# Kernel optimization log

Measured on AMD Instinct MI355X. Metric: run time of the kernel, lower is better.

The kernel has to match this reference:

```python
import jax, jax.numpy as jnp
import numpy as np

B, K, D = 32768, 32, 128

def setup_inputs() -> dict:
    key = jax.random.key(0)
    k1, k2, k3, k4, k5, k6 = jax.random.split(key, 6)
    s = 1.0 / np.sqrt(D)
    return {
        "h_ego": jax.random.normal(k1, (B, D), jnp.float32),
        "h_nei": jax.random.normal(k2, (B, K, D), jnp.float32),
        "nbr_mask": jax.random.randint(k3, (B, K), 0, 2, jnp.int32),
        "W_msg": jax.random.normal(k4, (D, D), jnp.float32) * s,
        "W_attn": jax.random.normal(k5, (1, 2 * D), jnp.float32) * s,
        "W_self": jax.random.normal(k6, (D, D), jnp.float32) * s,
        "b_self": jnp.zeros((D,), jnp.float32),
    }

def reference(h_ego, h_nei, nbr_mask, W_msg, W_attn, W_self, b_self):
    # msg_proj (nn.Linear, no bias): y = x @ W.T
    nbr_proj = jnp.einsum('bkd,ed->bke', h_nei, W_msg)          # [B,K,D]
    ego_proj = jnp.einsum('bd,ed->be', h_ego, W_msg)            # [B,D]
    # additive scorer on [ego_proj || nbr_proj]: split W_attn into two halves
    a = W_attn[0]                                               # [2D]
    a_ego, a_nbr = a[:D], a[D:]
    logits = ego_proj @ a_ego[:, None]                          # [B,1]
    logits = logits + jnp.einsum('bkd,d->bk', nbr_proj, a_nbr)  # [B,K]
    logits = jax.nn.leaky_relu(logits, negative_slope=0.2)
    logits = jnp.where(nbr_mask > 0, logits, -jnp.inf)
    attn = jax.nn.softmax(logits, axis=1)                       # [B,K]
    attn = jnp.where(jnp.isfinite(attn), attn, 0.0)
    nbr_message = jnp.einsum('bkd,bk->bd', nbr_proj, attn)      # [B,D]
    self_loop = h_ego @ W_self.T + b_self                       # [B,D]
    return jnp.tanh(nbr_message + self_loop)
```

## Files before the change

kernel.cpp:

```cpp
#include <hip/hip_runtime.h>
#include <hip/hip_bf16.h>
#include <math.h>

#define B_ROWS 32768
#define KNBR 32
#define DDIM 128

#define WS_VEGO 0
#define WS_VNBR 128
#define WS_WMT  256
#define WS_WST  (256 + 128*128)

__global__ __launch_bounds__(256) void prep_kernel(
    const float* __restrict__ W_msg, const float* __restrict__ W_attn,
    const float* __restrict__ W_self, float* __restrict__ ws) {
    int t = threadIdx.x;
    int gid = blockIdx.x * 256 + t;
    if (gid < 128 * 128) {
        int e = gid >> 7, d = gid & 127;
        ws[WS_WMT + d * 128 + e] = W_msg[e * 128 + d];
        ws[WS_WST + d * 128 + e] = W_self[e * 128 + d];
    }
    if (blockIdx.x == 0 && t < 128) {
        float ve = 0.f, vn = 0.f;
        for (int e = 0; e < 128; ++e) {
            float w = W_msg[e * 128 + t];
            ve += W_attn[e] * w;
            vn += W_attn[128 + e] * w;
        }
        ws[WS_VEGO + t] = ve;
        ws[WS_VNBR + t] = vn;
    }
}

__global__ __launch_bounds__(256) void attn_kernel(
    const float* __restrict__ h_ego, const float* __restrict__ h_nei,
    const int* __restrict__ nbr_mask, const float* __restrict__ ws,
    float* __restrict__ hbar_out) {
    __shared__ float hn[KNBR * DDIM];
    __shared__ float he[DDIM];
    __shared__ float sve[DDIM];
    __shared__ float svn[DDIM];
    __shared__ float s_raw[KNBR];
    __shared__ float s_attn[KNBR];
    __shared__ float s_ego;

    int t = threadIdx.x;
    long b = blockIdx.x;

    const float4* src = (const float4*)(h_nei + b * (KNBR * DDIM));
    float4* dst = (float4*)hn;
#pragma unroll
    for (int i = 0; i < 4; ++i) dst[i * 256 + t] = src[i * 256 + t];
    if (t < 32) {
        ((float4*)he)[t] = ((const float4*)(h_ego + b * DDIM))[t];
    } else if (t < 64) {
        ((float4*)sve)[t - 32] = ((const float4*)(ws + WS_VEGO))[t - 32];
    } else if (t < 96) {
        ((float4*)svn)[t - 64] = ((const float4*)(ws + WS_VNBR))[t - 64];
    }
    __syncthreads();

    int w = t >> 6, l = t & 63;

    if (w == 0) {
        float p = he[l] * sve[l] + he[l + 64] * sve[l + 64];
#pragma unroll
        for (int s = 32; s; s >>= 1) p += __shfl_xor(p, s, 64);
        if (l == 0) s_ego = p;
    }
#pragma unroll
    for (int j = 0; j < 8; ++j) {
        int k = w * 8 + j;
        const float* row = hn + k * DDIM;
        float p = row[l] * svn[l] + row[l + 64] * svn[l + 64];
#pragma unroll
        for (int s = 32; s; s >>= 1) p += __shfl_xor(p, s, 64);
        if (l == 0) s_raw[k] = p;
    }
    __syncthreads();

    if (w == 0) {
        float logit = -INFINITY;
        bool valid = false;
        if (l < KNBR) {
            float x = s_raw[l] + s_ego;
            x = x > 0.f ? x : 0.2f * x;
            valid = nbr_mask[b * KNBR + l] > 0;
            logit = valid ? x : -INFINITY;
        }
        float m = logit;
#pragma unroll
        for (int s = 32; s; s >>= 1) m = fmaxf(m, __shfl_xor(m, s, 64));
        float e = valid ? __expf(logit - m) : 0.f;
        float ssum = e;
#pragma unroll
        for (int s = 32; s; s >>= 1) ssum += __shfl_xor(ssum, s, 64);
        if (l < KNBR) s_attn[l] = (ssum > 0.f) ? e / ssum : 0.f;
    }
    __syncthreads();

    if (t < DDIM) {
        float acc = 0.f;
#pragma unroll
        for (int k = 0; k < KNBR; ++k) acc += s_attn[k] * hn[k * DDIM + t];
        hbar_out[b * DDIM + t] = acc;
    }
}

__global__ __launch_bounds__(256) void out_kernel(
    const float* __restrict__ h_ego, const float* __restrict__ ws,
    const float* __restrict__ b_self, float* __restrict__ out) {
    __shared__ float xh[32 * DDIM];
    __shared__ float xe[32 * DDIM];

    int t = threadIdx.x;
    long rbase = (long)blockIdx.x * 32;

    const float4* srcH = (const float4*)(out + rbase * DDIM);
    const float4* srcE = (const float4*)(h_ego + rbase * DDIM);
#pragma unroll
    for (int i = 0; i < 4; ++i) {
        ((float4*)xh)[i * 256 + t] = srcH[i * 256 + t];
        ((float4*)xe)[i * 256 + t] = srcE[i * 256 + t];
    }
    __syncthreads();

    const float4* WmT = (const float4*)(ws + WS_WMT);
    const float4* WsT = (const float4*)(ws + WS_WST);
    int tc = t & 31;
    int tr = t >> 5;

    float acc[4][4] = {{0.f}};
    for (int d = 0; d < 128; ++d) {
        float4 wm = WmT[d * 32 + tc];
        float4 wsv = WsT[d * 32 + tc];
#pragma unroll
        for (int r = 0; r < 4; ++r) {
            float a = xh[(tr * 4 + r) * DDIM + d];
            float bb = xe[(tr * 4 + r) * DDIM + d];
            acc[r][0] += a * wm.x + bb * wsv.x;
            acc[r][1] += a * wm.y + bb * wsv.y;
            acc[r][2] += a * wm.z + bb * wsv.z;
            acc[r][3] += a * wm.w + bb * wsv.w;
        }
    }

    float4 bv = ((const float4*)b_self)[tc];
#pragma unroll
    for (int r = 0; r < 4; ++r) {
        float4 o;
        o.x = tanhf(acc[r][0] + bv.x);
        o.y = tanhf(acc[r][1] + bv.y);
        o.z = tanhf(acc[r][2] + bv.z);
        o.w = tanhf(acc[r][3] + bv.w);
        ((float4*)(out + (rbase + tr * 4 + r) * DDIM))[tc] = o;
    }
}

extern "C" void kernel_launch(void* const* d_in, const int* in_sizes, int n_in,
                              void* d_out, int out_size, void* d_ws, size_t ws_size,
                              hipStream_t stream) {
    const float* h_ego   = (const float*)d_in[0];
    const float* h_nei   = (const float*)d_in[1];
    const int*   nbr_mask= (const int*)d_in[2];
    const float* W_msg   = (const float*)d_in[3];
    const float* W_attn  = (const float*)d_in[4];
    const float* W_self  = (const float*)d_in[5];
    const float* b_self  = (const float*)d_in[6];
    float* out = (float*)d_out;
    float* ws  = (float*)d_ws;

    prep_kernel<<<64, 256, 0, stream>>>(W_msg, W_attn, W_self, ws);
    attn_kernel<<<B_ROWS, 256, 0, stream>>>(h_ego, h_nei, nbr_mask, ws, out);
    out_kernel<<<B_ROWS / 32, 256, 0, stream>>>(h_ego, ws, b_self, out);
}
```

Measured before the change: 764.9 us.

## Process one batch row per wavefront with register-resident neighbor tiles

The attention kernel now maps one wavefront to each batch row, four rows per block, instead of one 256-thread block per row. Each lane keeps its float2 slice of all 32 neighbor rows in registers, so the shared-memory staging and the three block-wide barriers go away. The mask is read through a wavefront ballot, and the softmax runs redundantly in every lane. This cuts LDS traffic and synchronization but raises register pressure (64 floats for neighbors plus 32 for exponentials), which may lower occupancy. The kernel is memory-bound on h_nei, so the gain depends on whether the loads stay well in flight.

```diff
diff --git a/kernel.cpp b/kernel.cpp
--- a/kernel.cpp
+++ b/kernel.cpp
@@ -37,75 +37,58 @@
     const float* __restrict__ h_ego, const float* __restrict__ h_nei,
     const int* __restrict__ nbr_mask, const float* __restrict__ ws,
     float* __restrict__ hbar_out) {
-    __shared__ float hn[KNBR * DDIM];
-    __shared__ float he[DDIM];
-    __shared__ float sve[DDIM];
-    __shared__ float svn[DDIM];
-    __shared__ float s_raw[KNBR];
-    __shared__ float s_attn[KNBR];
-    __shared__ float s_ego;
+    int t = threadIdx.x;
+    int w = t >> 6, l = t & 63;
+    long b = (long)blockIdx.x * 4 + w;
 
-    int t = threadIdx.x;
-    long b = blockIdx.x;
+    float2 vn2 = ((const float2*)(ws + WS_VNBR))[l];
+    float2 ve2 = ((const float2*)(ws + WS_VEGO))[l];
+    float2 he2 = ((const float2*)(h_ego + b * DDIM))[l];
 
-    const float4* src = (const float4*)(h_nei + b * (KNBR * DDIM));
-    float4* dst = (float4*)hn;
+    const float2* row = (const float2*)(h_nei + b * (KNBR * DDIM));
+    float2 hreg[KNBR];
 #pragma unroll
-    for (int i = 0; i < 4; ++i) dst[i * 256 + t] = src[i * 256 + t];
-    if (t < 32) {
-        ((float4*)he)[t] = ((const float4*)(h_ego + b * DDIM))[t];
-    } else if (t < 64) {
-        ((float4*)sve)[t - 32] = ((const float4*)(ws + WS_VEGO))[t - 32];
-    } else if (t < 96) {
-        ((float4*)svn)[t - 64] = ((const float4*)(ws + WS_VNBR))[t - 64];
-    }
-    __syncthreads();
+    for (int k = 0; k < KNBR; ++k) hreg[k] = row[k * 64 + l];
 
-    int w = t >> 6, l = t & 63;
+    int mv = nbr_mask[b * KNBR + (l & 31)];
+    unsigned long long bal = __ballot((l < KNBR) && (mv > 0));
+    unsigned vmask = (unsigned)bal;
 
-    if (w == 0) {
-        float p = he[l] * sve[l] + he[l + 64] * sve[l + 64];
+    float pe = he2.x * ve2.x + he2.y * ve2.y;
+#pragma unroll
+    for (int s = 32; s; s >>= 1) pe += __shfl_xor(pe, s, 64);
+
+    float e[KNBR];
+    float m = -INFINITY;
+#pragma unroll
+    for (int k = 0; k < KNBR; ++k) {
+        float p = hreg[k].x * vn2.x + hreg[k].y * vn2.y;
 #pragma unroll
         for (int s = 32; s; s >>= 1) p += __shfl_xor(p, s, 64);
-        if (l == 0) s_ego = p;
+        p += pe;
+        p = p > 0.f ? p : 0.2f * p;
+        p = ((vmask >> k) & 1u) ? p : -INFINITY;
+        e[k] = p;
+        m = fmaxf(m, p);
     }
+    float ssum = 0.f;
 #pragma unroll
-    for (int j = 0; j < 8; ++j) {
-        int k = w * 8 + j;
-        const float* row = hn + k * DDIM;
-        float p = row[l] * svn[l] + row[l + 64] * svn[l + 64];
+    for (int k = 0; k < KNBR; ++k) {
+        float ev = ((vmask >> k) & 1u) ? __expf(e[k] - m) : 0.f;
+        e[k] = ev;
+        ssum += ev;
+    }
+    float inv = ssum > 0.f ? 1.f / ssum : 0.f;
+
+    float2 acc = make_float2(0.f, 0.f);
 #pragma unroll
-        for (int s = 32; s; s >>= 1) p += __shfl_xor(p, s, 64);
-        if (l == 0) s_raw[k] = p;
+    for (int k = 0; k < KNBR; ++k) {
+        acc.x += e[k] * hreg[k].x;
+        acc.y += e[k] * hreg[k].y;
     }
-    __syncthreads();
-
-    if (w == 0) {
-        float logit = -INFINITY;
-        bool valid = false;
-        if (l < KNBR) {
-            float x = s_raw[l] + s_ego;
-            x = x > 0.f ? x : 0.2f * x;
-            valid = nbr_mask[b * KNBR + l] > 0;
-            logit = valid ? x : -INFINITY;
-        }
-        float m = logit;
-#pragma unroll
-        for (int s = 32; s; s >>= 1) m = fmaxf(m, __shfl_xor(m, s, 64));
-        float e = valid ? __expf(logit - m) : 0.f;
-        float ssum = e;
-#pragma unroll
-        for (int s = 32; s; s >>= 1) ssum += __shfl_xor(ssum, s, 64);
-        if (l < KNBR) s_attn[l] = (ssum > 0.f) ? e / ssum : 0.f;
-    }
-    __syncthreads();
-
-    if (t < DDIM) {
-        float acc = 0.f;
-#pragma unroll
-        for (int k = 0; k < KNBR; ++k) acc += s_attn[k] * hn[k * DDIM + t];
-        hbar_out[b * DDIM + t] = acc;
-    }
+    acc.x *= inv;
+    acc.y *= inv;
+    ((float2*)(hbar_out + b * DDIM))[l] = acc;
 }
 
 __global__ __launch_bounds__(256) void out_kernel(
@@ -172,6 +155,6 @@
     float* ws  = (float*)d_ws;
 
     prep_kernel<<<64, 256, 0, stream>>>(W_msg, W_attn, W_self, ws);
-    attn_kernel<<<B_ROWS, 256, 0, stream>>>(h_ego, h_nei, nbr_mask, ws, out);
+    attn_kernel<<<B_ROWS / 4, 256, 0, stream>>>(h_ego, h_nei, nbr_mask, ws, out);
     out_kernel<<<B_ROWS / 32, 256, 0, stream>>>(h_ego, ws, b_self, out);
 }
```

Measured after the change: 755.9 us. About the same (-1.2%).
